# Performance work log

Hardware: AMD Instinct MI355X
Metric: run time of the kernel (lower is better)

## Reference

```python
import jax, jax.numpy as jnp
import numpy as np

D_MODEL = 1024
N_HEADS = 16
HEAD_DIM = D_MODEL // N_HEADS


def setup_inputs() -> dict:
    key = jax.random.key(0)
    k1, k2, k3 = jax.random.split(key, 3)
    x = jax.random.normal(k1, (4, 2048, D_MODEL), dtype=jnp.float32)
    # torch Linear weight is [out, in]; y = x @ W.T
    w_qkv = jax.random.normal(k2, (3 * D_MODEL, D_MODEL), dtype=jnp.float32) * (1.0 / np.sqrt(D_MODEL))
    w_proj = jax.random.normal(k3, (D_MODEL, D_MODEL), dtype=jnp.float32) * (1.0 / np.sqrt(D_MODEL))
    return {"x": x, "w_qkv": w_qkv, "w_proj": w_proj}


def reference(x, w_qkv, w_proj):
    B, T, C = x.shape
    qkv = jnp.einsum('btc,oc->bto', x, w_qkv)  # [B,T,3C]
    q, k, v = jnp.split(qkv, 3, axis=-1)
    # [B,T,H,D] -> [B,H,T,D]
    def to_heads(t):
        return t.reshape(B, T, N_HEADS, HEAD_DIM).transpose(0, 2, 1, 3)
    q, k, v = to_heads(q), to_heads(k), to_heads(v)
    scale = 1.0 / np.sqrt(HEAD_DIM).astype(np.float32)
    scores = jnp.einsum('bhqd,bhkd->bhqk', q, k) * scale  # [B,H,T,T]
    causal = jnp.tril(jnp.ones((T, T), dtype=bool))
    scores = jnp.where(causal, scores, jnp.finfo(scores.dtype).min)
    attn = jax.nn.softmax(scores, axis=-1)
    out = jnp.einsum('bhqk,bhkd->bhqd', attn, v)  # [B,H,T,D]
    out = out.transpose(0, 2, 1, 3).reshape(B, T, C)
    return jnp.einsum('btc,oc->bto', out, w_proj)
```

## Files before the change

### kernel.cpp

```cpp
#include <hip/hip_runtime.h>

#define B_ 4
#define T_ 2048
#define C_ 1024
#define H_ 16
#define D_ 64

typedef __bf16 bf16;
typedef bf16 bf16x8 __attribute__((ext_vector_type(8)));
typedef bf16 bf16x4v __attribute__((ext_vector_type(4)));
typedef float f32x4 __attribute__((ext_vector_type(4)));

__device__ __forceinline__ int probe_is_f32(const void* p, int lane) {
  float v = fminf(fabsf((float)((const bf16*)p)[lane]), 100.f);
#pragma unroll
  for (int o = 1; o < 64; o <<= 1) v += __shfl_xor(v, o, 64);
  return v > 300.f ? 1 : 0;
}

__device__ __forceinline__ void gload16(const void* g, void* l) {
  __builtin_amdgcn_global_load_lds(
      (const __attribute__((address_space(1))) void*)g,
      (__attribute__((address_space(3))) void*)l, 16, 0, 0);
}

__global__ __launch_bounds__(256) void cvt_bf16(const void* __restrict__ src,
                                                size_t elofs,
                                                bf16* __restrict__ dst,
                                                int n8) {
  if (!probe_is_f32(src, threadIdx.x & 63)) return;
  int i = blockIdx.x * 256 + threadIdx.x;
  if (i >= n8) return;
  const float* s = (const float*)src + elofs + (size_t)i * 8;
  f32x4 u0 = *(const f32x4*)s;
  f32x4 u1 = *(const f32x4*)(s + 4);
  bf16x8 o;
#pragma unroll
  for (int j = 0; j < 4; ++j) { o[j] = (bf16)u0[j]; o[4 + j] = (bf16)u1[j]; }
  *(bf16x8*)(dst + (size_t)i * 8) = o;
}

__global__ __launch_bounds__(256) void transpose_o(const bf16* __restrict__ src,
                                                   bf16* __restrict__ dst) {
  int i = blockIdx.x * 256 + threadIdx.x;
  int d8 = i & 7;
  int r = i >> 3;
  int t = r & (T_ - 1);
  int r2 = r >> 11;
  int h = r2 & (H_ - 1);
  int b = r2 >> 4;
  bf16x8 v =
      *(const bf16x8*)(src + ((size_t)(b * H_ + h) * T_ + t) * D_ + d8 * 8);
  *(bf16x8*)(dst + ((size_t)(b * T_ + t) * C_) + h * D_ + d8 * 8) = v;
}

__global__ __launch_bounds__(256, 3) void gemm_bt(
    const void* __restrict__ A, const bf16* __restrict__ Ab, int arowbase,
    int tmofs, const void* __restrict__ W, const bf16* __restrict__ Wcvt,
    int M, int N, int K, int amode, int omode, void* __restrict__ out,
    bf16* __restrict__ qb, bf16* __restrict__ kb, bf16* __restrict__ vtb,
    const void* __restrict__ px, const void* __restrict__ pwq,
    const void* __restrict__ pwp, int bsel) {
  __shared__ __align__(16) char lds[16384];
  char* ldsA = lds;
  char* ldsB = lds + 8192;

  const int ntiles = N >> 7;
  int bid = blockIdx.x;
  if ((gridDim.x & 7) == 0) {
    int cpx = gridDim.x >> 3;
    bid = (bid & 7) * cpx + (bid >> 3);
  }
  const int tm = tmofs + bid / ntiles;
  const int tn = bid % ntiles;
  const int tid = threadIdx.x;
  const int lane = tid & 63;
  const int wv = tid >> 6;
  const int wm = wv >> 1, wn = wv & 1;
  const int lm = lane & 15, lq = lane >> 4;

  const int fx = probe_is_f32(px, lane);
  const int fwq = probe_is_f32(pwq, lane);
  const int fwp = probe_is_f32(pwp, lane);
  const int outF32 = fx | fwq | fwp;
  const int bF32 = bsel ? fwp : fwq;
  const bf16* Wb = bF32 ? Wcvt : (const bf16*)W;
  const bf16* Asrc = (amode == 0 && fx) ? Ab : (const bf16*)A;
  const int rowadj = (amode == 0 && fx) ? arowbase : 0;

  size_t boff[2];
#pragma unroll
  for (int h = 0; h < 2; ++h) {
    int c = tid + h * 256, rbk = c >> 6, ll = c & 63;
    boff[h] = (size_t)(tn * 128 + rbk * 16 + (ll & 15)) * K + (ll >> 4) * 8;
  }
  size_t aoffb[2];
  int ab2[2], at2[2], acq[2];
#pragma unroll
  for (int h = 0; h < 2; ++h) {
    int c = tid + h * 256, rbk = c >> 6, ll = c & 63;
    int row = tm * 128 + rbk * 16 + (ll & 15);
    aoffb[h] = (size_t)(row - rowadj) * K + (ll >> 4) * 8;
    ab2[h] = row >> 11;
    at2[h] = row & 2047;
    acq[h] = ll >> 4;
  }

  f32x4 acc[4][4] = {};

  for (int k0 = 0; k0 < K; k0 += 32) {
    __syncthreads();
    if (amode == 2) {
#pragma unroll
      for (int h = 0; h < 2; ++h) {
        int kk = k0 + acq[h] * 8;
        size_t off =
            ((size_t)(ab2[h] * H_ + (kk >> 6)) * T_ + at2[h]) * D_ + (kk & 63);
        gload16((const bf16*)A + off, ldsA + (tid + h * 256) * 16);
      }
    } else {
#pragma unroll
      for (int h = 0; h < 2; ++h)
        gload16(Asrc + aoffb[h] + k0, ldsA + (tid + h * 256) * 16);
    }
#pragma unroll
    for (int h = 0; h < 2; ++h)
      gload16(Wb + boff[h] + k0, ldsB + (tid + h * 256) * 16);
    __syncthreads();

    bf16x8 af[4], bff[4];
#pragma unroll
    for (int i = 0; i < 4; ++i)
      af[i] = *(const bf16x8*)(ldsA + (wm * 4 + i) * 1024 + lane * 16);
#pragma unroll
    for (int j = 0; j < 4; ++j)
      bff[j] = *(const bf16x8*)(ldsB + (wn * 4 + j) * 1024 + lane * 16);
#pragma unroll
    for (int i = 0; i < 4; ++i)
#pragma unroll
      for (int j = 0; j < 4; ++j)
        acc[i][j] = __builtin_amdgcn_mfma_f32_16x16x32_bf16(af[i], bff[j],
                                                            acc[i][j], 0, 0, 0);
  }

  if (omode == 0) {
#pragma unroll
    for (int i = 0; i < 4; ++i) {
      int row0 = tm * 128 + wm * 64 + i * 16 + lq * 4;
#pragma unroll
      for (int j = 0; j < 4; ++j) {
        int col = tn * 128 + wn * 64 + j * 16 + lm;
#pragma unroll
        for (int r = 0; r < 4; ++r) {
          size_t idx = (size_t)(row0 + r) * N + col;
          if (outF32) ((float*)out)[idx] = acc[i][j][r];
          else        ((bf16*)out)[idx]  = (bf16)acc[i][j][r];
        }
      }
    }
  } else {
#pragma unroll
    for (int j = 0; j < 4; ++j) {
      int o = tn * 128 + wn * 64 + j * 16 + lm;
      int which = o >> 10;
      int c = o & 1023;
      int h = c >> 6, d = c & 63;
#pragma unroll
      for (int i = 0; i < 4; ++i) {
        int row0 = tm * 128 + wm * 64 + i * 16 + lq * 4;
        int b = row0 >> 11, t0 = row0 & 2047;
        if (which == 2) {
          bf16x4v pk;
#pragma unroll
          for (int r = 0; r < 4; ++r) pk[r] = (bf16)acc[i][j][r];
          *(bf16x4v*)(vtb + ((size_t)((b * H_ + h) * D_ + d)) * T_ + t0) = pk;
        } else {
          bf16* dst = (which == 0) ? qb : kb;
#pragma unroll
          for (int r = 0; r < 4; ++r)
            dst[((size_t)((b * H_ + h) * T_ + t0 + r)) * D_ + d] =
                (bf16)acc[i][j][r];
        }
      }
    }
  }
}

__global__ __launch_bounds__(256, 4) void attn_fwd(bf16* __restrict__ Q,
                                                   const bf16* __restrict__ Kk,
                                                   const bf16* __restrict__ Vt) {
  __shared__ __align__(16) char lds[12288];
  char* ldsK = lds;
  char* ldsV = lds + 4096;
  char* ldsP = lds + 8192;

  const int tid = threadIdx.x;
  const int bh = blockIdx.x & 63;
  const int pi = blockIdx.x >> 6;
  const int lane = tid & 63;
  const int wv = tid >> 6;
  const int lm = lane & 15, lq = lane >> 4;

  const int kRow = (wv >> 1) * 16 + lm;
  const int kD = (wv & 1) * 32 + lq * 8;
  const int vD = wv * 16 + lm;

  const bf16* ksrc = Kk + ((size_t)(bh * T_ + kRow)) * D_ + kD;
  const bf16* vsrc = Vt + ((size_t)(bh * D_ + vD)) * T_ + lq * 8;
  char* myP = ldsP + wv * 1024;

  bf16x8 vones;
#pragma unroll
  for (int j = 0; j < 8; ++j) vones[j] = (bf16)1.0f;

#pragma unroll 1
  for (int phase = 0; phase < 2; ++phase) {
    const int qt = phase ? (31 - pi) : pi;
    const int q0w = qt * 64 + wv * 16;

    bf16x8 qa[2];
    {
      const bf16* qbase = Q + ((size_t)(bh * T_ + q0w + lm)) * D_ + lq * 8;
      qa[0] = *(const bf16x8*)(qbase);
      qa[1] = *(const bf16x8*)(qbase + 32);
    }

    f32x4 oacc[4] = {};
    f32x4 lacc = {};
    const int jend = qt * 64 + 64;

    for (int j0 = 0; j0 < jend; j0 += 32) {
      __syncthreads();
      gload16(ksrc + (size_t)j0 * D_, ldsK + tid * 16);
      gload16(vsrc + j0, ldsV + tid * 16);
      __syncthreads();

      bf16x8 kf[2][2], vf[4];
#pragma unroll
      for (int t = 0; t < 2; ++t)
#pragma unroll
        for (int kc = 0; kc < 2; ++kc)
          kf[t][kc] = *(const bf16x8*)(ldsK + (t * 2 + kc) * 1024 + lane * 16);
#pragma unroll
      for (int nt = 0; nt < 4; ++nt)
        vf[nt] = *(const bf16x8*)(ldsV + nt * 1024 + lane * 16);

#pragma unroll
      for (int t = 0; t < 2; ++t) {
        f32x4 s = {};
        s = __builtin_amdgcn_mfma_f32_16x16x32_bf16(qa[0], kf[t][0], s, 0, 0, 0);
        s = __builtin_amdgcn_mfma_f32_16x16x32_bf16(qa[1], kf[t][1], s, 0, 0, 0);
        int kcol = j0 + t * 16 + lm;
        int chunkc = t * 2 + (lm >> 3);
        int jj = lm & 7;
        char* pdst = myP + (chunkc * 16 + lq * 4) * 16 + jj * 2;
        if (j0 + t * 16 + 15 <= q0w) {
#pragma unroll
          for (int r = 0; r < 4; ++r) {
            bf16 pb = (bf16)__expf(s[r] * 0.125f);
            *(bf16*)(pdst + r * 16) = pb;
          }
        } else {
#pragma unroll
          for (int r = 0; r < 4; ++r) {
            int qrow = q0w + lq * 4 + r;
            float p = (kcol <= qrow) ? __expf(s[r] * 0.125f) : 0.0f;
            *(bf16*)(pdst + r * 16) = (bf16)p;
          }
        }
      }
      bf16x8 pf = *(const bf16x8*)(myP + lane * 16);
      lacc = __builtin_amdgcn_mfma_f32_16x16x32_bf16(pf, vones, lacc, 0, 0, 0);
#pragma unroll
      for (int nt = 0; nt < 4; ++nt)
        oacc[nt] = __builtin_amdgcn_mfma_f32_16x16x32_bf16(pf, vf[nt], oacc[nt],
                                                            0, 0, 0);
    }

    float rinv[4];
#pragma unroll
    for (int r = 0; r < 4; ++r) rinv[r] = 1.0f / fmaxf(lacc[r], 1e-30f);
#pragma unroll
    for (int nt = 0; nt < 4; ++nt)
#pragma unroll
      for (int r = 0; r < 4; ++r) {
        int t = q0w + lq * 4 + r;
        Q[((size_t)(bh * T_ + t)) * D_ + nt * 16 + lm] =
            (bf16)(oacc[nt][r] * rinv[r]);
      }
  }
}

extern "C" void kernel_launch(void* const* d_in, const int* in_sizes, int n_in,
                              void* d_out, int out_size, void* d_ws,
                              size_t ws_size, hipStream_t stream) {
  const void* x = d_in[0];
  const void* wqkv = d_in[1];
  const void* wproj = d_in[2];

  const size_t NE = (size_t)B_ * T_ * C_;
  bf16* qb = (bf16*)d_ws;
  bf16* kb = qb + NE;
  bf16* vtb = (bf16*)d_out;
  bf16* wqkvb = vtb + NE;
  bf16* xb1 = wqkvb + 3 * C_ * C_;
  bf16* ob = kb;
  bf16* wprojb = qb;

  const int M = B_ * T_;
  const int Mh = M / 2;
  const int nh8 = Mh * C_ / 8;

  cvt_bf16<<<(3 * C_ * C_ / 8) / 256, 256, 0, stream>>>(wqkv, 0, wqkvb,
                                                        3 * C_ * C_ / 8);
  cvt_bf16<<<nh8 / 256, 256, 0, stream>>>(x, 0, xb1, nh8);
  gemm_bt<<<(Mh / 128) * (3 * C_ / 128), 256, 0, stream>>>(
      x, xb1, 0, 0, wqkv, wqkvb, M, 3 * C_, C_,
      0, 1, nullptr, qb, kb, vtb, x, wqkv, wproj,
      0);
  cvt_bf16<<<nh8 / 256, 256, 0, stream>>>(x, (size_t)Mh * C_, xb1, nh8);
  gemm_bt<<<(Mh / 128) * (3 * C_ / 128), 256, 0, stream>>>(
      x, xb1, Mh, Mh / 128, wqkv, wqkvb, M, 3 * C_, C_,
      0, 1, nullptr, qb, kb, vtb, x, wqkv, wproj,
      0);
  attn_fwd<<<(T_ / 64 / 2) * B_ * H_, 256, 0, stream>>>(qb, kb, vtb);
  transpose_o<<<(int)(NE / 8 / 256), 256, 0, stream>>>(qb, ob);
  cvt_bf16<<<(C_ * C_ / 8) / 256, 256, 0, stream>>>(wproj, 0, wprojb,
                                                    C_ * C_ / 8);
  gemm_bt<<<(M / 128) * (C_ / 128), 256, 0, stream>>>(
      ob, ob, 0, 0, wproj, wprojb, M, C_, C_,
      0, 0, d_out, nullptr, nullptr, nullptr, x, wqkv,
      wproj, 1);
}
```

Measured before the change: 311.4 us.

## Fuse fp32-to-bf16 conversion of x into QKV GEMM A-tile loads

The QKV GEMM now loads fp32 x tiles straight into LDS with a swizzled layout and converts them to bf16 while building MFMA fragments. This removes the separate x conversion kernels and the split of the QKV GEMM into two half-M launches, replacing them with one full launch. In exchange, A-tile LDS traffic and global reads double (fp32), LDS grows to 24KB per block, and conversion work is repeated by every N-tile block.

Measured after the change: 309.6 us. No clear change (-0.6%).

```diff
diff --git a/kernel.cpp b/kernel.cpp
--- a/kernel.cpp
+++ b/kernel.cpp
@@ -55,15 +55,14 @@
 }
 
 __global__ __launch_bounds__(256, 3) void gemm_bt(
-    const void* __restrict__ A, const bf16* __restrict__ Ab, int arowbase,
-    int tmofs, const void* __restrict__ W, const bf16* __restrict__ Wcvt,
-    int M, int N, int K, int amode, int omode, void* __restrict__ out,
-    bf16* __restrict__ qb, bf16* __restrict__ kb, bf16* __restrict__ vtb,
-    const void* __restrict__ px, const void* __restrict__ pwq,
-    const void* __restrict__ pwp, int bsel) {
-  __shared__ __align__(16) char lds[16384];
+    const void* __restrict__ A, const void* __restrict__ W,
+    const bf16* __restrict__ Wcvt, int M, int N, int K, int aprobe, int omode,
+    void* __restrict__ out, bf16* __restrict__ qb, bf16* __restrict__ kb,
+    bf16* __restrict__ vtb, const void* __restrict__ px,
+    const void* __restrict__ pwq, const void* __restrict__ pwp, int bsel) {
+  __shared__ __align__(16) char lds[24576];
   char* ldsA = lds;
-  char* ldsB = lds + 8192;
+  char* ldsB = lds + 16384;
 
   const int ntiles = N >> 7;
   int bid = blockIdx.x;
@@ -71,7 +70,7 @@
     int cpx = gridDim.x >> 3;
     bid = (bid & 7) * cpx + (bid >> 3);
   }
-  const int tm = tmofs + bid / ntiles;
+  const int tm = bid / ntiles;
   const int tn = bid % ntiles;
   const int tid = threadIdx.x;
   const int lane = tid & 63;
@@ -85,8 +84,7 @@
   const int outF32 = fx | fwq | fwp;
   const int bF32 = bsel ? fwp : fwq;
   const bf16* Wb = bF32 ? Wcvt : (const bf16*)W;
-  const bf16* Asrc = (amode == 0 && fx) ? Ab : (const bf16*)A;
-  const int rowadj = (amode == 0 && fx) ? arowbase : 0;
+  const int aF32 = aprobe ? fx : 0;
 
   size_t boff[2];
 #pragma unroll
@@ -94,34 +92,38 @@
     int c = tid + h * 256, rbk = c >> 6, ll = c & 63;
     boff[h] = (size_t)(tn * 128 + rbk * 16 + (ll & 15)) * K + (ll >> 4) * 8;
   }
+  size_t aofff[4];
   size_t aoffb[2];
-  int ab2[2], at2[2], acq[2];
-#pragma unroll
-  for (int h = 0; h < 2; ++h) {
-    int c = tid + h * 256, rbk = c >> 6, ll = c & 63;
-    int row = tm * 128 + rbk * 16 + (ll & 15);
-    aoffb[h] = (size_t)(row - rowadj) * K + (ll >> 4) * 8;
-    ab2[h] = row >> 11;
-    at2[h] = row & 2047;
-    acq[h] = ll >> 4;
+  if (aF32) {
+#pragma unroll
+    for (int h = 0; h < 4; ++h) {
+      int c = tid + h * 256;
+      int w = c >> 6;
+      int ln = c & 63;
+      int row = tm * 128 + w * 8 + (ln >> 3);
+      int kq = (ln & 7) ^ (ln >> 3);
+      aofff[h] = (size_t)row * K + kq * 4;
+    }
+  } else {
+#pragma unroll
+    for (int h = 0; h < 2; ++h) {
+      int c = tid + h * 256, rbk = c >> 6, ll = c & 63;
+      aoffb[h] = (size_t)(tm * 128 + rbk * 16 + (ll & 15)) * K + (ll >> 4) * 8;
+    }
   }
 
   f32x4 acc[4][4] = {};
 
   for (int k0 = 0; k0 < K; k0 += 32) {
     __syncthreads();
-    if (amode == 2) {
-#pragma unroll
-      for (int h = 0; h < 2; ++h) {
-        int kk = k0 + acq[h] * 8;
-        size_t off =
-            ((size_t)(ab2[h] * H_ + (kk >> 6)) * T_ + at2[h]) * D_ + (kk & 63);
-        gload16((const bf16*)A + off, ldsA + (tid + h * 256) * 16);
-      }
+    if (aF32) {
+#pragma unroll
+      for (int h = 0; h < 4; ++h)
+        gload16((const float*)A + aofff[h] + k0, ldsA + (tid + h * 256) * 16);
     } else {
 #pragma unroll
       for (int h = 0; h < 2; ++h)
-        gload16(Asrc + aoffb[h] + k0, ldsA + (tid + h * 256) * 16);
+        gload16((const bf16*)A + aoffb[h] + k0, ldsA + (tid + h * 256) * 16);
     }
 #pragma unroll
     for (int h = 0; h < 2; ++h)
@@ -129,9 +131,27 @@
     __syncthreads();
 
     bf16x8 af[4], bff[4];
-#pragma unroll
-    for (int i = 0; i < 4; ++i)
-      af[i] = *(const bf16x8*)(ldsA + (wm * 4 + i) * 1024 + lane * 16);
+    if (aF32) {
+      const int r7 = lm & 7;
+      const int hi = lm >> 3;
+      const int u0 = (2 * lq) ^ r7;
+      const int u1 = (2 * lq + 1) ^ r7;
+#pragma unroll
+      for (int i = 0; i < 4; ++i) {
+        const char* pbase = ldsA + (((wm * 4 + i) * 2 + hi) << 10) + r7 * 128;
+        f32x4 lo = *(const f32x4*)(pbase + u0 * 16);
+        f32x4 hh = *(const f32x4*)(pbase + u1 * 16);
+#pragma unroll
+        for (int j = 0; j < 4; ++j) {
+          af[i][j] = (bf16)lo[j];
+          af[i][4 + j] = (bf16)hh[j];
+        }
+      }
+    } else {
+#pragma unroll
+      for (int i = 0; i < 4; ++i)
+        af[i] = *(const bf16x8*)(ldsA + (wm * 4 + i) * 1024 + lane * 16);
+    }
 #pragma unroll
     for (int j = 0; j < 4; ++j)
       bff[j] = *(const bf16x8*)(ldsB + (wn * 4 + j) * 1024 + lane * 16);
@@ -303,32 +323,21 @@
   bf16* kb = qb + NE;
   bf16* vtb = (bf16*)d_out;
   bf16* wqkvb = vtb + NE;
-  bf16* xb1 = wqkvb + 3 * C_ * C_;
   bf16* ob = kb;
   bf16* wprojb = qb;
 
   const int M = B_ * T_;
-  const int Mh = M / 2;
-  const int nh8 = Mh * C_ / 8;
 
   cvt_bf16<<<(3 * C_ * C_ / 8) / 256, 256, 0, stream>>>(wqkv, 0, wqkvb,
                                                         3 * C_ * C_ / 8);
-  cvt_bf16<<<nh8 / 256, 256, 0, stream>>>(x, 0, xb1, nh8);
-  gemm_bt<<<(Mh / 128) * (3 * C_ / 128), 256, 0, stream>>>(
-      x, xb1, 0, 0, wqkv, wqkvb, M, 3 * C_, C_,
-      0, 1, nullptr, qb, kb, vtb, x, wqkv, wproj,
-      0);
-  cvt_bf16<<<nh8 / 256, 256, 0, stream>>>(x, (size_t)Mh * C_, xb1, nh8);
-  gemm_bt<<<(Mh / 128) * (3 * C_ / 128), 256, 0, stream>>>(
-      x, xb1, Mh, Mh / 128, wqkv, wqkvb, M, 3 * C_, C_,
-      0, 1, nullptr, qb, kb, vtb, x, wqkv, wproj,
-      0);
+  gemm_bt<<<(M / 128) * (3 * C_ / 128), 256, 0, stream>>>(
+      x, wqkv, wqkvb, M, 3 * C_, C_, 1, 1, nullptr, qb,
+      kb, vtb, x, wqkv, wproj, 0);
   attn_fwd<<<(T_ / 64 / 2) * B_ * H_, 256, 0, stream>>>(qb, kb, vtb);
   transpose_o<<<(int)(NE / 8 / 256), 256, 0, stream>>>(qb, ob);
   cvt_bf16<<<(C_ * C_ / 8) / 256, 256, 0, stream>>>(wproj, 0, wprojb,
                                                     C_ * C_ / 8);
   gemm_bt<<<(M / 128) * (C_ / 128), 256, 0, stream>>>(
-      ob, ob, 0, 0, wproj, wprojb, M, C_, C_,
-      0, 0, d_out, nullptr, nullptr, nullptr, x, wqkv,
-      wproj, 1);
-}
+      ob, wproj, wprojb, M, C_, C_, 0, 0, d_out, nullptr,
+      nullptr, nullptr, x, wqkv, wproj, 1);
+}
```
